# Kernel optimization log

Measured on AMD Instinct MI355X. Metric: run time of the kernel, lower is better.

## Reference

```python
import jax, jax.numpy as jnp
import numpy as np

N_NODES = 50000
N_EDGES = 800000
N_HEADS = 8
MULT = 16  # multiplicity per degree
F_KEY_NFEAT = MULT * 1 + MULT * 3  # 64


def setup_inputs() -> dict:
    key = jax.random.key(0)
    ks = jax.random.split(key, 7)
    return {
        "v0": jax.random.normal(ks[0], (N_EDGES, MULT, 1), dtype=jnp.float32),
        "v1": jax.random.normal(ks[1], (N_EDGES, MULT, 3), dtype=jnp.float32),
        "k0": jax.random.normal(ks[2], (N_EDGES, MULT, 1), dtype=jnp.float32),
        "k1": jax.random.normal(ks[3], (N_EDGES, MULT, 3), dtype=jnp.float32),
        "q0": jax.random.normal(ks[4], (N_NODES, MULT, 1), dtype=jnp.float32),
        "q1": jax.random.normal(ks[5], (N_NODES, MULT, 3), dtype=jnp.float32),
        "edge_index": jax.random.randint(ks[6], (2, N_EDGES), 0, N_NODES, dtype=jnp.int32),
    }


def _fiber2head(d0, d1, n_heads):
    # [X, m, 2d+1] -> [X, H, (m/H)*(2d+1)], concat over degrees on last axis
    x0 = d0.reshape(d0.shape[0], n_heads, -1)
    x1 = d1.reshape(d1.shape[0], n_heads, -1)
    return jnp.concatenate([x0, x1], axis=-1)


def reference(v0, v1, k0, k1, q0, q1, edge_index):
    row, col = edge_index[0], edge_index[1]
    N = q0.shape[0]
    H = N_HEADS

    k = _fiber2head(k0, k1, H)          # [E, H, 8]
    q = _fiber2head(q0, q1, H)          # [N, H, 8]

    # per-edge attention logits (dot over channel dim), scaled by sqrt(f_key.n_features)
    e = (k * q[col]).sum(axis=2) / np.float32(np.sqrt(F_KEY_NFEAT))  # [E, H]
    e = jnp.exp(e)
    s = jax.ops.segment_sum(e, row, num_segments=N)  # [N, H]
    a = e / s[row]                                   # [E, H]
    attn = a[:, :, None, None]                       # [E, H, 1, 1]

    mH = MULT // H
    # degree-0 messages: [E, H, m/H, 1]
    out0 = jax.ops.segment_sum(attn * v0.reshape(-1, H, mH, 1), col, num_segments=N)
    out0 = out0.reshape(N, MULT, 1)
    # degree-1 messages: [E, H, m/H, 3]
    out1 = jax.ops.segment_sum(attn * v1.reshape(-1, H, mH, 3), col, num_segments=N)
    out1 = out1.reshape(N, MULT, 3)
    return out0, out1
```

## Files before the change

### kernel.cpp

```cpp
#include <hip/hip_runtime.h>
#include <hip/hip_fp16.h>

#define N_NODES 50000
#define N_EDGES 800000

struct alignas(16) H8 { __half h[8]; };

__global__ __launch_bounds__(256) void k_hist(const int* __restrict__ ei,
                                              int* __restrict__ cnt_r,
                                              int* __restrict__ cnt_c)
{
    int e = blockIdx.x * blockDim.x + threadIdx.x;
    if (e >= N_EDGES) return;
    atomicAdd(cnt_r + ei[e], 1);
    atomicAdd(cnt_c + ei[N_EDGES + e], 1);
}

#define SCAN_T 1024
#define SCAN_I 8
__global__ __launch_bounds__(SCAN_T) void k_scan2(int* cnt_r, int* off_r,
                                                  int* cnt_c, int* off_c)
{
    __shared__ int sm[SCAN_T];
    __shared__ int carry_s;
    const int n = N_NODES;
    for (int pass = 0; pass < 2; ++pass) {
        int* cnt = pass ? cnt_c : cnt_r;
        int* off = pass ? off_c : off_r;
        if (threadIdx.x == 0) carry_s = 0;
        __syncthreads();
        for (int base = 0; base < n; base += SCAN_T * SCAN_I) {
            int idx0 = base + threadIdx.x * SCAN_I;
            int v[SCAN_I];
            int sum = 0;
            #pragma unroll
            for (int j = 0; j < SCAN_I; ++j) {
                int i = idx0 + j;
                v[j] = (i < n) ? cnt[i] : 0;
                sum += v[j];
            }
            sm[threadIdx.x] = sum;
            __syncthreads();
            for (int d = 1; d < SCAN_T; d <<= 1) {
                int t = (threadIdx.x >= d) ? sm[threadIdx.x - d] : 0;
                __syncthreads();
                sm[threadIdx.x] += t;
                __syncthreads();
            }
            int excl_thread = sm[threadIdx.x] - sum;
            int carry = carry_s;
            int run = carry + excl_thread;
            #pragma unroll
            for (int j = 0; j < SCAN_I; ++j) {
                int i = idx0 + j;
                if (i < n) { off[i] = run; cnt[i] = run; }
                run += v[j];
            }
            __syncthreads();
            if (threadIdx.x == SCAN_T - 1) carry_s = carry + sm[threadIdx.x];
            __syncthreads();
        }
        if (threadIdx.x == 0) off[n] = carry_s;
        __syncthreads();
    }
}

__global__ __launch_bounds__(256) void k_logits_fill(
    const float* __restrict__ k0, const float* __restrict__ k1,
    const float* __restrict__ q0, const float* __restrict__ q1,
    const int* __restrict__ ei, __half* __restrict__ e_buf,
    int* __restrict__ cur_r, int* __restrict__ cur_c,
    int* __restrict__ eid_r, int* __restrict__ eid_c)
{
    int e = blockIdx.x * blockDim.x + threadIdx.x;
    if (e >= N_EDGES) return;
    int row = ei[e];
    int col = ei[N_EDGES + e];

    int pr = atomicAdd(cur_r + row, 1);
    int pc = atomicAdd(cur_c + col, 1);

    const float4* k0v = (const float4*)(k0 + (size_t)e   * 16);
    const float4* q0v = (const float4*)(q0 + (size_t)col * 16);
    const float4* k1v = (const float4*)(k1 + (size_t)e   * 48);
    const float4* q1v = (const float4*)(q1 + (size_t)col * 48);

    float acc[8];
    #pragma unroll
    for (int h = 0; h < 8; ++h) acc[h] = 0.f;

    #pragma unroll
    for (int i = 0; i < 4; ++i) {
        float4 kv = k0v[i];
        float4 qv = q0v[i];
        acc[(4*i+0)/2] += kv.x * qv.x;
        acc[(4*i+1)/2] += kv.y * qv.y;
        acc[(4*i+2)/2] += kv.z * qv.z;
        acc[(4*i+3)/2] += kv.w * qv.w;
    }
    #pragma unroll
    for (int j = 0; j < 12; ++j) {
        float4 kv = k1v[j];
        float4 qv = q1v[j];
        acc[(4*j+0)/6] += kv.x * qv.x;
        acc[(4*j+1)/6] += kv.y * qv.y;
        acc[(4*j+2)/6] += kv.z * qv.z;
        acc[(4*j+3)/6] += kv.w * qv.w;
    }

    H8 pack;
    #pragma unroll
    for (int h = 0; h < 8; ++h) pack.h[h] = __float2half(__expf(acc[h] * 0.125f));
    *(H8*)(e_buf + (size_t)e * 8) = pack;

    eid_r[pr] = e;
    eid_c[pc] = e;
}

__global__ __launch_bounds__(256) void k_s(const __half* __restrict__ e_buf,
                                           const int* __restrict__ off_r,
                                           const int* __restrict__ eid_r,
                                           float* __restrict__ rs)
{
    int t = blockIdx.x * blockDim.x + threadIdx.x;
    int node = t >> 3;
    int h = t & 7;
    if (node >= N_NODES) return;
    int beg = off_r[node], end = off_r[node + 1];
    float acc = 0.f;
    int i = beg;
    for (; i + 4 <= end; i += 4) {
        int e0 = eid_r[i + 0];
        int e1 = eid_r[i + 1];
        int e2 = eid_r[i + 2];
        int e3 = eid_r[i + 3];
        float x0 = __half2float(e_buf[(size_t)e0 * 8 + h]);
        float x1 = __half2float(e_buf[(size_t)e1 * 8 + h]);
        float x2 = __half2float(e_buf[(size_t)e2 * 8 + h]);
        float x3 = __half2float(e_buf[(size_t)e3 * 8 + h]);
        acc += x0; acc += x1; acc += x2; acc += x3;
    }
    for (; i < end; ++i) {
        acc += __half2float(e_buf[(size_t)eid_r[i] * 8 + h]);
    }
    rs[(size_t)node * 8 + h] = 1.0f / acc;
}

__global__ __launch_bounds__(256) void k_out(
    const float* __restrict__ v0, const float* __restrict__ v1,
    const int* __restrict__ ei, const __half* __restrict__ e_buf,
    const float* __restrict__ rs,
    const int* __restrict__ off_c, const int* __restrict__ eid_c,
    float* __restrict__ out0, float* __restrict__ out1)
{
    int wave = (blockIdx.x * blockDim.x + threadIdx.x) >> 6;
    int lane = threadIdx.x & 63;
    if (wave >= N_NODES) return;
    bool is0 = lane < 16;
    int f1 = lane - 16;
    int head = is0 ? (lane >> 1) : (f1 / 6);
    const float* __restrict__ vbase = is0 ? (v0 + lane) : (v1 + f1);
    int vstride = is0 ? 16 : 48;

    int beg = off_c[wave], end = off_c[wave + 1];
    float acc = 0.f;
    int i = beg;
    for (; i + 4 <= end; i += 4) {
        int e0 = eid_c[i + 0];
        int e1 = eid_c[i + 1];
        int e2 = eid_c[i + 2];
        int e3 = eid_c[i + 3];
        int r0 = ei[e0], r1 = ei[e1], r2 = ei[e2], r3 = ei[e3];
        float w0 = vbase[(size_t)e0 * vstride];
        float w1 = vbase[(size_t)e1 * vstride];
        float w2 = vbase[(size_t)e2 * vstride];
        float w3 = vbase[(size_t)e3 * vstride];
        float a0 = __half2float(e_buf[(size_t)e0 * 8 + head]) * rs[(size_t)r0 * 8 + head];
        float a1 = __half2float(e_buf[(size_t)e1 * 8 + head]) * rs[(size_t)r1 * 8 + head];
        float a2 = __half2float(e_buf[(size_t)e2 * 8 + head]) * rs[(size_t)r2 * 8 + head];
        float a3 = __half2float(e_buf[(size_t)e3 * 8 + head]) * rs[(size_t)r3 * 8 + head];
        acc += a0 * w0;
        acc += a1 * w1;
        acc += a2 * w2;
        acc += a3 * w3;
    }
    for (; i < end; ++i) {
        int e0 = eid_c[i];
        int r0 = ei[e0];
        acc += __half2float(e_buf[(size_t)e0 * 8 + head])
             * rs[(size_t)r0 * 8 + head]
             * vbase[(size_t)e0 * vstride];
    }
    if (is0) out0[(size_t)wave * 16 + lane] = acc;
    else     out1[(size_t)wave * 48 + f1]   = acc;
}

extern "C" void kernel_launch(void* const* d_in, const int* in_sizes, int n_in,
                              void* d_out, int out_size, void* d_ws, size_t ws_size,
                              hipStream_t stream) {
    const float* v0 = (const float*)d_in[0];
    const float* v1 = (const float*)d_in[1];
    const float* k0 = (const float*)d_in[2];
    const float* k1 = (const float*)d_in[3];
    const float* q0 = (const float*)d_in[4];
    const float* q1 = (const float*)d_in[5];
    const int*   ei = (const int*)d_in[6];

    float* out0 = (float*)d_out;
    float* out1 = out0 + (size_t)N_NODES * 16;

    char* ws = (char*)d_ws;
    int*    cnt_r = (int*)   (ws + 0);
    int*    cnt_c = (int*)   (ws + 200000);
    int*    off_r = (int*)   (ws + 400000);
    int*    off_c = (int*)   (ws + 600016);
    int*    eid_r = (int*)   (ws + 800032);
    int*    eid_c = (int*)   (ws + 4000032);
    __half* e_buf = (__half*)(ws + 7200032);
    float*  rs    = (float*) (ws + 20000032);

    hipMemsetAsync(cnt_r, 0, 400000, stream);

    const int block = 256;
    const int gridE = (N_EDGES + block - 1) / block;

    k_hist<<<gridE, block, 0, stream>>>(ei, cnt_r, cnt_c);
    k_scan2<<<1, SCAN_T, 0, stream>>>(cnt_r, off_r, cnt_c, off_c);
    k_logits_fill<<<gridE, block, 0, stream>>>(k0, k1, q0, q1, ei, e_buf,
                                               cnt_r, cnt_c, eid_r, eid_c);
    k_s<<<(N_NODES * 8 + block - 1) / block, block, 0, stream>>>(e_buf, off_r, eid_r, rs);
    k_out<<<(N_NODES * 64 + block - 1) / block, block, 0, stream>>>(
        v0, v1, ei, e_buf, rs, off_c, eid_c, out0, out1);
}
```

Measured before the change: 734.2 us.

## Parallelize scan across two blocks, pack row with column edge ids, add nontemporal loads

The two prefix scans now run concurrently in two blocks, each using wave shuffles instead of a shared-memory Hillis-Steele loop with many barriers. The column-sorted edge list now stores (edge, row) pairs, so k_out no longer does a dependent gather of ei. Streaming k and v reads use nontemporal loads, and the gather loops are unrolled to 8 for more memory-level parallelism. In exchange, the column edge list doubles in size and its writes get wider, and the workspace layout shifts.

After: 744.8 us. No clear change (+1.4%).

```diff
diff --git a/kernel.cpp b/kernel.cpp
--- a/kernel.cpp
+++ b/kernel.cpp
@@ -5,6 +5,7 @@
 #define N_EDGES 800000
 
 struct alignas(16) H8 { __half h[8]; };
+typedef float vfloat4 __attribute__((ext_vector_type(4)));
 
 __global__ __launch_bounds__(256) void k_hist(const int* __restrict__ ei,
                                               int* __restrict__ cnt_r,
@@ -21,48 +22,55 @@
 __global__ __launch_bounds__(SCAN_T) void k_scan2(int* cnt_r, int* off_r,
                                                   int* cnt_c, int* off_c)
 {
-    __shared__ int sm[SCAN_T];
+    int* cnt = blockIdx.x ? cnt_c : cnt_r;
+    int* off = blockIdx.x ? off_c : off_r;
+    __shared__ int wsum[16];
     __shared__ int carry_s;
     const int n = N_NODES;
-    for (int pass = 0; pass < 2; ++pass) {
-        int* cnt = pass ? cnt_c : cnt_r;
-        int* off = pass ? off_c : off_r;
-        if (threadIdx.x == 0) carry_s = 0;
-        __syncthreads();
-        for (int base = 0; base < n; base += SCAN_T * SCAN_I) {
-            int idx0 = base + threadIdx.x * SCAN_I;
-            int v[SCAN_I];
-            int sum = 0;
+    int wid = threadIdx.x >> 6, lane = threadIdx.x & 63;
+    if (threadIdx.x == 0) carry_s = 0;
+    __syncthreads();
+    for (int base = 0; base < n; base += SCAN_T * SCAN_I) {
+        int idx0 = base + threadIdx.x * SCAN_I;
+        int v[SCAN_I];
+        int sum = 0;
+        #pragma unroll
+        for (int j = 0; j < SCAN_I; ++j) {
+            int i = idx0 + j;
+            v[j] = (i < n) ? cnt[i] : 0;
+            sum += v[j];
+        }
+        int x = sum;
+        #pragma unroll
+        for (int d = 1; d < 64; d <<= 1) {
+            int t = __shfl_up(x, d);
+            if (lane >= d) x += t;
+        }
+        if (lane == 63) wsum[wid] = x;
+        __syncthreads();
+        if (wid == 0 && lane < 16) {
+            int y = wsum[lane];
             #pragma unroll
-            for (int j = 0; j < SCAN_I; ++j) {
-                int i = idx0 + j;
-                v[j] = (i < n) ? cnt[i] : 0;
-                sum += v[j];
+            for (int d = 1; d < 16; d <<= 1) {
+                int t = __shfl_up(y, d);
+                if (lane >= d) y += t;
             }
-            sm[threadIdx.x] = sum;
-            __syncthreads();
-            for (int d = 1; d < SCAN_T; d <<= 1) {
-                int t = (threadIdx.x >= d) ? sm[threadIdx.x - d] : 0;
-                __syncthreads();
-                sm[threadIdx.x] += t;
-                __syncthreads();
-            }
-            int excl_thread = sm[threadIdx.x] - sum;
-            int carry = carry_s;
-            int run = carry + excl_thread;
-            #pragma unroll
-            for (int j = 0; j < SCAN_I; ++j) {
-                int i = idx0 + j;
-                if (i < n) { off[i] = run; cnt[i] = run; }
-                run += v[j];
-            }
-            __syncthreads();
-            if (threadIdx.x == SCAN_T - 1) carry_s = carry + sm[threadIdx.x];
-            __syncthreads();
-        }
-        if (threadIdx.x == 0) off[n] = carry_s;
-        __syncthreads();
-    }
+            wsum[lane] = y;
+        }
+        __syncthreads();
+        int wave_excl = wid ? wsum[wid - 1] : 0;
+        int run = carry_s + wave_excl + (x - sum);
+        #pragma unroll
+        for (int j = 0; j < SCAN_I; ++j) {
+            int i = idx0 + j;
+            if (i < n) { off[i] = run; cnt[i] = run; }
+            run += v[j];
+        }
+        __syncthreads();
+        if (threadIdx.x == 0) carry_s += wsum[15];
+        __syncthreads();
+    }
+    if (threadIdx.x == 0) off[n] = carry_s;
 }
 
 __global__ __launch_bounds__(256) void k_logits_fill(
@@ -70,7 +78,7 @@
     const float* __restrict__ q0, const float* __restrict__ q1,
     const int* __restrict__ ei, __half* __restrict__ e_buf,
     int* __restrict__ cur_r, int* __restrict__ cur_c,
-    int* __restrict__ eid_r, int* __restrict__ eid_c)
+    int* __restrict__ eid_r, int2* __restrict__ eid_c2)
 {
     int e = blockIdx.x * blockDim.x + threadIdx.x;
     if (e >= N_EDGES) return;
@@ -80,10 +88,10 @@
     int pr = atomicAdd(cur_r + row, 1);
     int pc = atomicAdd(cur_c + col, 1);
 
-    const float4* k0v = (const float4*)(k0 + (size_t)e   * 16);
-    const float4* q0v = (const float4*)(q0 + (size_t)col * 16);
-    const float4* k1v = (const float4*)(k1 + (size_t)e   * 48);
-    const float4* q1v = (const float4*)(q1 + (size_t)col * 48);
+    const vfloat4* k0v = (const vfloat4*)(k0 + (size_t)e   * 16);
+    const float4*  q0v = (const float4*)(q0 + (size_t)col * 16);
+    const vfloat4* k1v = (const vfloat4*)(k1 + (size_t)e   * 48);
+    const float4*  q1v = (const float4*)(q1 + (size_t)col * 48);
 
     float acc[8];
     #pragma unroll
@@ -91,8 +99,8 @@
 
     #pragma unroll
     for (int i = 0; i < 4; ++i) {
-        float4 kv = k0v[i];
-        float4 qv = q0v[i];
+        vfloat4 kv = __builtin_nontemporal_load(k0v + i);
+        float4  qv = q0v[i];
         acc[(4*i+0)/2] += kv.x * qv.x;
         acc[(4*i+1)/2] += kv.y * qv.y;
         acc[(4*i+2)/2] += kv.z * qv.z;
@@ -100,8 +108,8 @@
     }
     #pragma unroll
     for (int j = 0; j < 12; ++j) {
-        float4 kv = k1v[j];
-        float4 qv = q1v[j];
+        vfloat4 kv = __builtin_nontemporal_load(k1v + j);
+        float4  qv = q1v[j];
         acc[(4*j+0)/6] += kv.x * qv.x;
         acc[(4*j+1)/6] += kv.y * qv.y;
         acc[(4*j+2)/6] += kv.z * qv.z;
@@ -114,7 +122,8 @@
     *(H8*)(e_buf + (size_t)e * 8) = pack;
 
     eid_r[pr] = e;
-    eid_c[pc] = e;
+    int2 pr2; pr2.x = e; pr2.y = row;
+    eid_c2[pc] = pr2;
 }
 
 __global__ __launch_bounds__(256) void k_s(const __half* __restrict__ e_buf,
@@ -129,16 +138,16 @@
     int beg = off_r[node], end = off_r[node + 1];
     float acc = 0.f;
     int i = beg;
-    for (; i + 4 <= end; i += 4) {
-        int e0 = eid_r[i + 0];
-        int e1 = eid_r[i + 1];
-        int e2 = eid_r[i + 2];
-        int e3 = eid_r[i + 3];
-        float x0 = __half2float(e_buf[(size_t)e0 * 8 + h]);
-        float x1 = __half2float(e_buf[(size_t)e1 * 8 + h]);
-        float x2 = __half2float(e_buf[(size_t)e2 * 8 + h]);
-        float x3 = __half2float(e_buf[(size_t)e3 * 8 + h]);
-        acc += x0; acc += x1; acc += x2; acc += x3;
+    for (; i + 8 <= end; i += 8) {
+        float x0 = __half2float(e_buf[(size_t)eid_r[i + 0] * 8 + h]);
+        float x1 = __half2float(e_buf[(size_t)eid_r[i + 1] * 8 + h]);
+        float x2 = __half2float(e_buf[(size_t)eid_r[i + 2] * 8 + h]);
+        float x3 = __half2float(e_buf[(size_t)eid_r[i + 3] * 8 + h]);
+        float x4 = __half2float(e_buf[(size_t)eid_r[i + 4] * 8 + h]);
+        float x5 = __half2float(e_buf[(size_t)eid_r[i + 5] * 8 + h]);
+        float x6 = __half2float(e_buf[(size_t)eid_r[i + 6] * 8 + h]);
+        float x7 = __half2float(e_buf[(size_t)eid_r[i + 7] * 8 + h]);
+        acc += ((x0 + x1) + (x2 + x3)) + ((x4 + x5) + (x6 + x7));
     }
     for (; i < end; ++i) {
         acc += __half2float(e_buf[(size_t)eid_r[i] * 8 + h]);
@@ -148,9 +157,8 @@
 
 __global__ __launch_bounds__(256) void k_out(
     const float* __restrict__ v0, const float* __restrict__ v1,
-    const int* __restrict__ ei, const __half* __restrict__ e_buf,
-    const float* __restrict__ rs,
-    const int* __restrict__ off_c, const int* __restrict__ eid_c,
+    const __half* __restrict__ e_buf, const float* __restrict__ rs,
+    const int* __restrict__ off_c, const int2* __restrict__ eid_c2,
     float* __restrict__ out0, float* __restrict__ out1)
 {
     int wave = (blockIdx.x * blockDim.x + threadIdx.x) >> 6;
@@ -165,31 +173,54 @@
     int beg = off_c[wave], end = off_c[wave + 1];
     float acc = 0.f;
     int i = beg;
+    for (; i + 8 <= end; i += 8) {
+        int2 p0 = eid_c2[i + 0];
+        int2 p1 = eid_c2[i + 1];
+        int2 p2 = eid_c2[i + 2];
+        int2 p3 = eid_c2[i + 3];
+        int2 p4 = eid_c2[i + 4];
+        int2 p5 = eid_c2[i + 5];
+        int2 p6 = eid_c2[i + 6];
+        int2 p7 = eid_c2[i + 7];
+        float w0 = __builtin_nontemporal_load(vbase + (size_t)p0.x * vstride);
+        float w1 = __builtin_nontemporal_load(vbase + (size_t)p1.x * vstride);
+        float w2 = __builtin_nontemporal_load(vbase + (size_t)p2.x * vstride);
+        float w3 = __builtin_nontemporal_load(vbase + (size_t)p3.x * vstride);
+        float w4 = __builtin_nontemporal_load(vbase + (size_t)p4.x * vstride);
+        float w5 = __builtin_nontemporal_load(vbase + (size_t)p5.x * vstride);
+        float w6 = __builtin_nontemporal_load(vbase + (size_t)p6.x * vstride);
+        float w7 = __builtin_nontemporal_load(vbase + (size_t)p7.x * vstride);
+        float a0 = __half2float(e_buf[(size_t)p0.x * 8 + head]) * rs[(size_t)p0.y * 8 + head];
+        float a1 = __half2float(e_buf[(size_t)p1.x * 8 + head]) * rs[(size_t)p1.y * 8 + head];
+        float a2 = __half2float(e_buf[(size_t)p2.x * 8 + head]) * rs[(size_t)p2.y * 8 + head];
+        float a3 = __half2float(e_buf[(size_t)p3.x * 8 + head]) * rs[(size_t)p3.y * 8 + head];
+        float a4 = __half2float(e_buf[(size_t)p4.x * 8 + head]) * rs[(size_t)p4.y * 8 + head];
+        float a5 = __half2float(e_buf[(size_t)p5.x * 8 + head]) * rs[(size_t)p5.y * 8 + head];
+        float a6 = __half2float(e_buf[(size_t)p6.x * 8 + head]) * rs[(size_t)p6.y * 8 + head];
+        float a7 = __half2float(e_buf[(size_t)p7.x * 8 + head]) * rs[(size_t)p7.y * 8 + head];
+        acc += a0 * w0; acc += a1 * w1; acc += a2 * w2; acc += a3 * w3;
+        acc += a4 * w4; acc += a5 * w5; acc += a6 * w6; acc += a7 * w7;
+    }
     for (; i + 4 <= end; i += 4) {
-        int e0 = eid_c[i + 0];
-        int e1 = eid_c[i + 1];
-        int e2 = eid_c[i + 2];
-        int e3 = eid_c[i + 3];
-        int r0 = ei[e0], r1 = ei[e1], r2 = ei[e2], r3 = ei[e3];
-        float w0 = vbase[(size_t)e0 * vstride];
-        float w1 = vbase[(size_t)e1 * vstride];
-        float w2 = vbase[(size_t)e2 * vstride];
-        float w3 = vbase[(size_t)e3 * vstride];
-        float a0 = __half2float(e_buf[(size_t)e0 * 8 + head]) * rs[(size_t)r0 * 8 + head];
-        float a1 = __half2float(e_buf[(size_t)e1 * 8 + head]) * rs[(size_t)r1 * 8 + head];
-        float a2 = __half2float(e_buf[(size_t)e2 * 8 + head]) * rs[(size_t)r2 * 8 + head];
-        float a3 = __half2float(e_buf[(size_t)e3 * 8 + head]) * rs[(size_t)r3 * 8 + head];
-        acc += a0 * w0;
-        acc += a1 * w1;
-        acc += a2 * w2;
-        acc += a3 * w3;
+        int2 p0 = eid_c2[i + 0];
+        int2 p1 = eid_c2[i + 1];
+        int2 p2 = eid_c2[i + 2];
+        int2 p3 = eid_c2[i + 3];
+        float w0 = __builtin_nontemporal_load(vbase + (size_t)p0.x * vstride);
+        float w1 = __builtin_nontemporal_load(vbase + (size_t)p1.x * vstride);
+        float w2 = __builtin_nontemporal_load(vbase + (size_t)p2.x * vstride);
+        float w3 = __builtin_nontemporal_load(vbase + (size_t)p3.x * vstride);
+        float a0 = __half2float(e_buf[(size_t)p0.x * 8 + head]) * rs[(size_t)p0.y * 8 + head];
+        float a1 = __half2float(e_buf[(size_t)p1.x * 8 + head]) * rs[(size_t)p1.y * 8 + head];
+        float a2 = __half2float(e_buf[(size_t)p2.x * 8 + head]) * rs[(size_t)p2.y * 8 + head];
+        float a3 = __half2float(e_buf[(size_t)p3.x * 8 + head]) * rs[(size_t)p3.y * 8 + head];
+        acc += a0 * w0; acc += a1 * w1; acc += a2 * w2; acc += a3 * w3;
     }
     for (; i < end; ++i) {
-        int e0 = eid_c[i];
-        int r0 = ei[e0];
-        acc += __half2float(e_buf[(size_t)e0 * 8 + head])
-             * rs[(size_t)r0 * 8 + head]
-             * vbase[(size_t)e0 * vstride];
+        int2 p0 = eid_c2[i];
+        acc += __half2float(e_buf[(size_t)p0.x * 8 + head])
+             * rs[(size_t)p0.y * 8 + head]
+             * __builtin_nontemporal_load(vbase + (size_t)p0.x * vstride);
     }
     if (is0) out0[(size_t)wave * 16 + lane] = acc;
     else     out1[(size_t)wave * 48 + f1]   = acc;
@@ -210,14 +241,14 @@
     float* out1 = out0 + (size_t)N_NODES * 16;
 
     char* ws = (char*)d_ws;
-    int*    cnt_r = (int*)   (ws + 0);
-    int*    cnt_c = (int*)   (ws + 200000);
-    int*    off_r = (int*)   (ws + 400000);
-    int*    off_c = (int*)   (ws + 600016);
-    int*    eid_r = (int*)   (ws + 800032);
-    int*    eid_c = (int*)   (ws + 4000032);
-    __half* e_buf = (__half*)(ws + 7200032);
-    float*  rs    = (float*) (ws + 20000032);
+    int*    cnt_r  = (int*)   (ws + 0);
+    int*    cnt_c  = (int*)   (ws + 200000);
+    int*    off_r  = (int*)   (ws + 400000);
+    int*    off_c  = (int*)   (ws + 600016);
+    int*    eid_r  = (int*)   (ws + 800032);
+    int2*   eid_c2 = (int2*)  (ws + 4000032);
+    __half* e_buf  = (__half*)(ws + 10400032);
+    float*  rs     = (float*) (ws + 23200032);
 
     hipMemsetAsync(cnt_r, 0, 400000, stream);
 
@@ -225,10 +256,10 @@
     const int gridE = (N_EDGES + block - 1) / block;
 
     k_hist<<<gridE, block, 0, stream>>>(ei, cnt_r, cnt_c);
-    k_scan2<<<1, SCAN_T, 0, stream>>>(cnt_r, off_r, cnt_c, off_c);
+    k_scan2<<<2, SCAN_T, 0, stream>>>(cnt_r, off_r, cnt_c, off_c);
     k_logits_fill<<<gridE, block, 0, stream>>>(k0, k1, q0, q1, ei, e_buf,
-                                               cnt_r, cnt_c, eid_r, eid_c);
+                                               cnt_r, cnt_c, eid_r, eid_c2);
     k_s<<<(N_NODES * 8 + block - 1) / block, block, 0, stream>>>(e_buf, off_r, eid_r, rs);
     k_out<<<(N_NODES * 64 + block - 1) / block, block, 0, stream>>>(
-        v0, v1, ei, e_buf, rs, off_c, eid_c, out0, out1);
-}
+        v0, v1, e_buf, rs, off_c, eid_c2, out0, out1);
+}
```
